# Kernel tuning notes

Hardware: AMD Instinct MI355X
Metric: run time of the kernel (lower is better)

Reference implementation:

```python
import jax, jax.numpy as jnp
import numpy as np

B, T, D, K = 256, 256, 768, 128  # batch, seq_len, num_dims, num_state


def setup_inputs() -> dict:
    key = jax.random.key(0)
    k1, k2, k3 = jax.random.split(key, 3)
    s = jax.random.normal(k1, (B, T, D), dtype=jnp.float32)          # embeddings
    means = jax.random.normal(k2, (K, D), dtype=jnp.float32)         # per-state Gaussian means
    var = jax.random.uniform(k3, (D,), dtype=jnp.float32,
                             minval=0.5, maxval=1.5)                  # shared diagonal variance
    return {"s": s, "means": means, "var": var}


def reference(s, means, var):
    """DMVFlow._eval_log_density: per-state diagonal-Gaussian log density.

    density[b,t,k] = -0.5*(D*log(2*pi) + sum_d log var[d])
                     -0.5*sum_d (s[b,t,d] - means[k,d])^2 / var[d]
    Expanded quadratic form so the k-contraction is a single GEMM instead of
    materializing a (B,T,K,D) broadcast.
    """
    d = s.shape[-1]
    inv_var = 1.0 / var                                              # (D,)
    log_norm = -0.5 * (d * jnp.log(2.0 * jnp.pi) + jnp.sum(jnp.log(var)))
    s2 = jnp.einsum('btd,d->bt', s * s, inv_var)                     # (B,T)
    cross = jnp.einsum('btd,kd->btk', s, means * inv_var)            # (B,T,K) GEMM
    m2 = jnp.einsum('kd,d->k', means * means, inv_var)               # (K,)
    quad = s2[..., None] - 2.0 * cross + m2                          # (B,T,K)
    return log_norm - 0.5 * quad
```

## Files before the change

### kernel.cpp

```cpp
#include <hip/hip_runtime.h>
#include <hip/hip_bf16.h>
#include <stdint.h>

#define D_DIM    768
#define K_STATES 128
#define M_ROWS   65536
#define BM       64
#define BK       32
#define NSTEPS   (D_DIM / BK)
#define LDSTRIDE 40

typedef __attribute__((ext_vector_type(8))) short bf16x8;
typedef __attribute__((ext_vector_type(4))) float f32x4;
typedef __attribute__((ext_vector_type(4))) int   i32x4;

__device__ __forceinline__ unsigned short f2bf(float f) {
    union { float f; unsigned u; } x; x.f = f;
    unsigned r = (x.u + 0x7FFFu + ((x.u >> 16) & 1u)) >> 16;
    return (unsigned short)r;
}

__global__ void __launch_bounds__(256) prep_kernel(
        const float* __restrict__ means, const float* __restrict__ var,
        unsigned short* __restrict__ mwbf, float* __restrict__ cvec) {
    const int k = blockIdx.x;
    const int t = threadIdx.x;
    float m2 = 0.f, ld = 0.f;
    for (int d = t; d < D_DIM; d += 256) {
        float v  = var[d];
        float iv = 1.0f / v;
        float m  = means[k * D_DIM + d];
        mwbf[k * D_DIM + d] = f2bf(m * iv);
        m2 += m * m * iv;
        ld += logf(v);
    }
#pragma unroll
    for (int off = 32; off > 0; off >>= 1) {
        m2 += __shfl_down(m2, off, 64);
        ld += __shfl_down(ld, off, 64);
    }
    __shared__ float rm[4], rl[4];
    const int wid = t >> 6;
    if ((t & 63) == 0) { rm[wid] = m2; rl[wid] = ld; }
    __syncthreads();
    if (t == 0) {
        float M2 = rm[0] + rm[1] + rm[2] + rm[3];
        float LD = rl[0] + rl[1] + rl[2] + rl[3];
        cvec[k] = -0.5f * ((float)D_DIM * 1.8378770664093453f + LD + M2);
    }
}

__global__ void __launch_bounds__(256, 4) dmv_main(
        const float* __restrict__ s, const unsigned short* __restrict__ mwbf,
        const float* __restrict__ var, const float* __restrict__ cvec,
        float* __restrict__ out) {
    __shared__ unsigned short As[2][BM * LDSTRIDE];
    __shared__ unsigned short Bs[2][K_STATES * LDSTRIDE];
    __shared__ float ivs[D_DIM];
    __shared__ float part[BM][8];
    __shared__ float s2row[BM];
    __shared__ float cs[K_STATES];

    const int t    = threadIdx.x;
    const int lane = t & 63;
    const int w    = t >> 6;
    const int wr   = w >> 1;
    const int wc   = w & 1;
    const long rowBase = (long)blockIdx.x * BM;

    for (int d = t; d < D_DIM; d += 256) ivs[d] = 1.0f / var[d];
    if (t < K_STATES) cs[t] = cvec[t];

    const int arow0 = t >> 3;
    const int acol  = (t & 7) * 4;
    const int brow0 = t >> 2;
    const int bcol  = (t & 3) * 8;

    const float*          sA = s    + (rowBase + arow0) * D_DIM + acol;
    const unsigned short* sB = mwbf + brow0 * D_DIM + bcol;

    f32x4 a0_[2], a1_[2];
    i32x4 b0_[2], b1_[2];
    float s2acc[2] = {0.f, 0.f};

    f32x4 acc[2][4];
#pragma unroll
    for (int i = 0; i < 2; ++i)
#pragma unroll
        for (int j = 0; j < 4; ++j) acc[i][j] = f32x4{0.f, 0.f, 0.f, 0.f};

#define LOADP(AP, BP, ST) do {                                                 \
    AP[0] = *(const f32x4*)(sA + (ST) * BK);                                   \
    AP[1] = *(const f32x4*)(sA + (long)32 * D_DIM + (ST) * BK);                \
    BP[0] = *(const i32x4*)(sB + (ST) * BK);                                   \
    BP[1] = *(const i32x4*)(sB + (long)64 * D_DIM + (ST) * BK);                \
} while (0)

#define STAGE(BUF, AP, BP, K0) do {                                            \
    f32x4 ivv = *reinterpret_cast<const f32x4*>(&ivs[(K0) + acol]);            \
    _Pragma("unroll")                                                          \
    for (int j = 0; j < 2; ++j) {                                              \
        const int row = j * 32 + arow0;                                        \
        f32x4 v = AP[j];                                                       \
        s2acc[j] += v[0]*v[0]*ivv[0] + v[1]*v[1]*ivv[1]                        \
                  + v[2]*v[2]*ivv[2] + v[3]*v[3]*ivv[3];                       \
        __hip_bfloat162 p0 = __float22bfloat162_rn(make_float2(v[0], v[1]));   \
        __hip_bfloat162 p1 = __float22bfloat162_rn(make_float2(v[2], v[3]));   \
        union { uint2 u2; __hip_bfloat162 h[2]; } pk;                          \
        pk.h[0] = p0; pk.h[1] = p1;                                            \
        *reinterpret_cast<uint2*>(&As[BUF][row * LDSTRIDE + acol]) = pk.u2;    \
    }                                                                          \
    _Pragma("unroll")                                                          \
    for (int j = 0; j < 2; ++j)                                                \
        *reinterpret_cast<i32x4*>(&Bs[BUF][(j * 64 + brow0) * LDSTRIDE + bcol])\
            = BP[j];                                                           \
} while (0)

    const int g  = (lane >> 4) * 8;
    const int rA = wr * 32 + (lane & 15);
    const int rB = wc * 64 + (lane & 15);

#define COMPUTE(BUF) do {                                                      \
    const unsigned short* Ab = &As[BUF][0];                                    \
    const unsigned short* Bb = &Bs[BUF][0];                                    \
    bf16x8 afrag[2], bfrag[4];                                                 \
    _Pragma("unroll")                                                          \
    for (int i = 0; i < 2; ++i)                                                \
        afrag[i] = *(const bf16x8*)(Ab + (rA + i * 16) * LDSTRIDE + g);        \
    _Pragma("unroll")                                                          \
    for (int j = 0; j < 4; ++j)                                                \
        bfrag[j] = *(const bf16x8*)(Bb + (rB + j * 16) * LDSTRIDE + g);        \
    _Pragma("unroll")                                                          \
    for (int i = 0; i < 2; ++i)                                                \
        _Pragma("unroll")                                                      \
        for (int j = 0; j < 4; ++j)                                            \
            acc[i][j] = __builtin_amdgcn_mfma_f32_16x16x32_bf16(               \
                            afrag[i], bfrag[j], acc[i][j], 0, 0, 0);           \
} while (0)

    LOADP(a0_, b0_, 0);
    LOADP(a1_, b1_, 1);
    __syncthreads();
    STAGE(0, a0_, b0_, 0);
    LOADP(a0_, b0_, 2);
    __syncthreads();

    for (int st = 0; st < NSTEPS; st += 2) {
        COMPUTE(0);
        STAGE(1, a1_, b1_, (st + 1) * BK);
        if (st + 3 < NSTEPS) LOADP(a1_, b1_, st + 3);
        __syncthreads();

        COMPUTE(1);
        if (st + 2 < NSTEPS) STAGE(0, a0_, b0_, (st + 2) * BK);
        if (st + 4 < NSTEPS) LOADP(a0_, b0_, st + 4);
        __syncthreads();
    }

#pragma unroll
    for (int j = 0; j < 2; ++j) part[j * 32 + arow0][t & 7] = s2acc[j];
    __syncthreads();
    if (t < BM) {
        float v = 0.f;
#pragma unroll
        for (int sl = 0; sl < 8; ++sl) v += part[t][sl];
        s2row[t] = v;
    }
    __syncthreads();

    const int colBase = wc * 64 + (lane & 15);
#pragma unroll
    for (int i = 0; i < 2; ++i) {
        const int rl0 = wr * 32 + i * 16 + (lane >> 4) * 4;
#pragma unroll
        for (int j = 0; j < 4; ++j) {
            const int col = colBase + j * 16;
            const float cj = cs[col];
#pragma unroll
            for (int r = 0; r < 4; ++r) {
                const int rl = rl0 + r;
                out[(rowBase + rl) * K_STATES + col] = acc[i][j][r] + cj - 0.5f * s2row[rl];
            }
        }
    }
#undef LOADP
#undef STAGE
#undef COMPUTE
}

extern "C" void kernel_launch(void* const* d_in, const int* in_sizes, int n_in,
                              void* d_out, int out_size, void* d_ws, size_t ws_size,
                              hipStream_t stream) {
    const float* s     = (const float*)d_in[0];
    const float* means = (const float*)d_in[1];
    const float* var   = (const float*)d_in[2];
    float* out = (float*)d_out;

    unsigned short* mwbf = (unsigned short*)d_ws;
    float* cvec = (float*)((char*)d_ws + (size_t)K_STATES * D_DIM * sizeof(unsigned short));

    prep_kernel<<<K_STATES, 256, 0, stream>>>(means, var, mwbf, cvec);
    dmv_main<<<M_ROWS / BM, 256, 0, stream>>>(s, mwbf, var, cvec, out);
}
```

Before: 46.02 us.

## Fuse means prep into GEMM kernel and single-buffer register prefetch

Removes the separate prep kernel. Each GEMM block now loads fp32 means directly, scales them by inverse variance, converts to bf16 in its staging step, and computes m2 and the log-variance constant itself. This saves a kernel launch and the workspace round trip. In exchange, all 1024 blocks redo the means scaling and read 4x more bytes for B (fp32 instead of bf16), and the prefetch depth drops from two register stages to one.

Result: slower. 52.98 us (+15.1%).

```diff
diff --git a/kernel.cpp b/kernel.cpp
--- a/kernel.cpp
+++ b/kernel.cpp
@@ -14,52 +14,16 @@
 typedef __attribute__((ext_vector_type(4))) float f32x4;
 typedef __attribute__((ext_vector_type(4))) int   i32x4;
 
-__device__ __forceinline__ unsigned short f2bf(float f) {
-    union { float f; unsigned u; } x; x.f = f;
-    unsigned r = (x.u + 0x7FFFu + ((x.u >> 16) & 1u)) >> 16;
-    return (unsigned short)r;
-}
-
-__global__ void __launch_bounds__(256) prep_kernel(
-        const float* __restrict__ means, const float* __restrict__ var,
-        unsigned short* __restrict__ mwbf, float* __restrict__ cvec) {
-    const int k = blockIdx.x;
-    const int t = threadIdx.x;
-    float m2 = 0.f, ld = 0.f;
-    for (int d = t; d < D_DIM; d += 256) {
-        float v  = var[d];
-        float iv = 1.0f / v;
-        float m  = means[k * D_DIM + d];
-        mwbf[k * D_DIM + d] = f2bf(m * iv);
-        m2 += m * m * iv;
-        ld += logf(v);
-    }
-#pragma unroll
-    for (int off = 32; off > 0; off >>= 1) {
-        m2 += __shfl_down(m2, off, 64);
-        ld += __shfl_down(ld, off, 64);
-    }
-    __shared__ float rm[4], rl[4];
-    const int wid = t >> 6;
-    if ((t & 63) == 0) { rm[wid] = m2; rl[wid] = ld; }
-    __syncthreads();
-    if (t == 0) {
-        float M2 = rm[0] + rm[1] + rm[2] + rm[3];
-        float LD = rl[0] + rl[1] + rl[2] + rl[3];
-        cvec[k] = -0.5f * ((float)D_DIM * 1.8378770664093453f + LD + M2);
-    }
-}
-
-__global__ void __launch_bounds__(256, 4) dmv_main(
-        const float* __restrict__ s, const unsigned short* __restrict__ mwbf,
-        const float* __restrict__ var, const float* __restrict__ cvec,
-        float* __restrict__ out) {
+__global__ void __launch_bounds__(256, 4) dmv_fused(
+        const float* __restrict__ s, const float* __restrict__ means,
+        const float* __restrict__ var, float* __restrict__ out) {
     __shared__ unsigned short As[2][BM * LDSTRIDE];
     __shared__ unsigned short Bs[2][K_STATES * LDSTRIDE];
     __shared__ float ivs[D_DIM];
     __shared__ float part[BM][8];
     __shared__ float s2row[BM];
     __shared__ float cs[K_STATES];
+    __shared__ float rlg[4];
 
     const int t    = threadIdx.x;
     const int lane = t & 63;
@@ -68,20 +32,28 @@
     const int wc   = w & 1;
     const long rowBase = (long)blockIdx.x * BM;
 
-    for (int d = t; d < D_DIM; d += 256) ivs[d] = 1.0f / var[d];
-    if (t < K_STATES) cs[t] = cvec[t];
+    float ldp = 0.f;
+    for (int d = t; d < D_DIM; d += 256) {
+        float v = var[d];
+        ivs[d] = 1.0f / v;
+        ldp += logf(v);
+    }
+#pragma unroll
+    for (int off = 32; off > 0; off >>= 1) ldp += __shfl_down(ldp, off, 64);
+    if ((t & 63) == 0) rlg[t >> 6] = ldp;
 
     const int arow0 = t >> 3;
     const int acol  = (t & 7) * 4;
-    const int brow0 = t >> 2;
-    const int bcol  = (t & 3) * 8;
+    const int brow  = t >> 1;
+    const int bcol0 = (t & 1) * 16;
 
-    const float*          sA = s    + (rowBase + arow0) * D_DIM + acol;
-    const unsigned short* sB = mwbf + brow0 * D_DIM + bcol;
+    const float* sA = s     + (rowBase + arow0) * D_DIM + acol;
+    const float* sM = means + brow * D_DIM + bcol0;
 
-    f32x4 a0_[2], a1_[2];
-    i32x4 b0_[2], b1_[2];
+    f32x4 aP[2];
+    f32x4 bP[4];
     float s2acc[2] = {0.f, 0.f};
+    float m2p = 0.f;
 
     f32x4 acc[2][4];
 #pragma unroll
@@ -89,31 +61,48 @@
 #pragma unroll
         for (int j = 0; j < 4; ++j) acc[i][j] = f32x4{0.f, 0.f, 0.f, 0.f};
 
-#define LOADP(AP, BP, ST) do {                                                 \
-    AP[0] = *(const f32x4*)(sA + (ST) * BK);                                   \
-    AP[1] = *(const f32x4*)(sA + (long)32 * D_DIM + (ST) * BK);                \
-    BP[0] = *(const i32x4*)(sB + (ST) * BK);                                   \
-    BP[1] = *(const i32x4*)(sB + (long)64 * D_DIM + (ST) * BK);                \
+#define LOADP(ST) do {                                                         \
+    aP[0] = *(const f32x4*)(sA + (ST) * BK);                                   \
+    aP[1] = *(const f32x4*)(sA + (long)32 * D_DIM + (ST) * BK);                \
+    bP[0] = *(const f32x4*)(sM + (ST) * BK);                                   \
+    bP[1] = *(const f32x4*)(sM + (ST) * BK + 4);                               \
+    bP[2] = *(const f32x4*)(sM + (ST) * BK + 8);                               \
+    bP[3] = *(const f32x4*)(sM + (ST) * BK + 12);                              \
 } while (0)
 
-#define STAGE(BUF, AP, BP, K0) do {                                            \
+#define STAGE(BUF, K0) do {                                                    \
+                                         \
     f32x4 ivv = *reinterpret_cast<const f32x4*>(&ivs[(K0) + acol]);            \
     _Pragma("unroll")                                                          \
     for (int j = 0; j < 2; ++j) {                                              \
         const int row = j * 32 + arow0;                                        \
-        f32x4 v = AP[j];                                                       \
+        f32x4 v = aP[j];                                                       \
         s2acc[j] += v[0]*v[0]*ivv[0] + v[1]*v[1]*ivv[1]                        \
                   + v[2]*v[2]*ivv[2] + v[3]*v[3]*ivv[3];                       \
-        __hip_bfloat162 p0 = __float22bfloat162_rn(make_float2(v[0], v[1]));   \
-        __hip_bfloat162 p1 = __float22bfloat162_rn(make_float2(v[2], v[3]));   \
         union { uint2 u2; __hip_bfloat162 h[2]; } pk;                          \
-        pk.h[0] = p0; pk.h[1] = p1;                                            \
+        pk.h[0] = __float22bfloat162_rn(make_float2(v[0], v[1]));              \
+        pk.h[1] = __float22bfloat162_rn(make_float2(v[2], v[3]));              \
         *reinterpret_cast<uint2*>(&As[BUF][row * LDSTRIDE + acol]) = pk.u2;    \
     }                                                                          \
-    _Pragma("unroll")                                                          \
-    for (int j = 0; j < 2; ++j)                                                \
-        *reinterpret_cast<i32x4*>(&Bs[BUF][(j * 64 + brow0) * LDSTRIDE + bcol])\
-            = BP[j];                                                           \
+                  \
+    {                                                                          \
+        union { i32x4 i4; __hip_bfloat162 h[4]; } q0, q1;                      \
+        _Pragma("unroll")                                                      \
+        for (int j = 0; j < 4; ++j) {                                          \
+            f32x4 iw = *reinterpret_cast<const f32x4*>(&ivs[(K0) + bcol0 + j*4]);\
+            f32x4 mv = bP[j];                                                  \
+            m2p += mv[0]*mv[0]*iw[0] + mv[1]*mv[1]*iw[1]                       \
+                 + mv[2]*mv[2]*iw[2] + mv[3]*mv[3]*iw[3];                      \
+            __hip_bfloat162 plo = __float22bfloat162_rn(                       \
+                make_float2(mv[0]*iw[0], mv[1]*iw[1]));                        \
+            __hip_bfloat162 phi = __float22bfloat162_rn(                       \
+                make_float2(mv[2]*iw[2], mv[3]*iw[3]));                        \
+            if (j < 2) { q0.h[(j&1)*2] = plo; q0.h[(j&1)*2+1] = phi; }         \
+            else       { q1.h[(j&1)*2] = plo; q1.h[(j&1)*2+1] = phi; }         \
+        }                                                                      \
+        *reinterpret_cast<i32x4*>(&Bs[BUF][brow * LDSTRIDE + bcol0])     = q0.i4;\
+        *reinterpret_cast<i32x4*>(&Bs[BUF][brow * LDSTRIDE + bcol0 + 8]) = q1.i4;\
+    }                                                                          \
 } while (0)
 
     const int g  = (lane >> 4) * 8;
@@ -138,27 +127,26 @@
                             afrag[i], bfrag[j], acc[i][j], 0, 0, 0);           \
 } while (0)
 
-    LOADP(a0_, b0_, 0);
-    LOADP(a1_, b1_, 1);
+    LOADP(0);
     __syncthreads();
-    STAGE(0, a0_, b0_, 0);
-    LOADP(a0_, b0_, 2);
-    __syncthreads();
+    const float slog = rlg[0] + rlg[1] + rlg[2] + rlg[3];
+    STAGE(0, 0);
 
-    for (int st = 0; st < NSTEPS; st += 2) {
-        COMPUTE(0);
-        STAGE(1, a1_, b1_, (st + 1) * BK);
-        if (st + 3 < NSTEPS) LOADP(a1_, b1_, st + 3);
+    for (int st = 0; st < NSTEPS; ++st) {
+        const int cur = st & 1;
+        if (st + 1 < NSTEPS) LOADP(st + 1);
         __syncthreads();
-
-        COMPUTE(1);
-        if (st + 2 < NSTEPS) STAGE(0, a0_, b0_, (st + 2) * BK);
-        if (st + 4 < NSTEPS) LOADP(a0_, b0_, st + 4);
-        __syncthreads();
+        COMPUTE(cur);
+        if (st + 1 < NSTEPS) STAGE(st + 1 & 1, (st + 1) * BK);
     }
 
 #pragma unroll
     for (int j = 0; j < 2; ++j) part[j * 32 + arow0][t & 7] = s2acc[j];
+    {
+        float m2t = m2p + __shfl_xor(m2p, 1, 64);
+        if (!(t & 1))
+            cs[brow] = -0.5f * ((float)D_DIM * 1.8378770664093453f + slog + m2t);
+    }
     __syncthreads();
     if (t < BM) {
         float v = 0.f;
@@ -196,9 +184,5 @@
     const float* var   = (const float*)d_in[2];
     float* out = (float*)d_out;
 
-    unsigned short* mwbf = (unsigned short*)d_ws;
-    float* cvec = (float*)((char*)d_ws + (size_t)K_STATES * D_DIM * sizeof(unsigned short));
-
-    prep_kernel<<<K_STATES, 256, 0, stream>>>(means, var, mwbf, cvec);
-    dmv_main<<<M_ROWS / BM, 256, 0, stream>>>(s, mwbf, var, cvec, out);
+    dmv_fused<<<M_ROWS / BM, 256, 0, stream>>>(s, means, var, out);
 }
```

## Double K-tile depth and simplify to one-barrier-per-step register prefetch pipeline

Applied to the files above, without the earlier changes.

Raises the reduction tile from 32 to 64 columns, with a padded LDS stride of 72. This halves the number of main-loop steps and barriers, and each COMPUTE now issues two MFMA k-substeps. The two-register-set prefetch scheme is replaced by a single prefetch buffer, one barrier per step, and a new thread-to-element mapping in which each thread loads four contiguous 16-byte chunks per row. Launch bounds drop from 4 to 2 blocks per SM, and the LDS footprint roughly doubles. On a kernel close to memory-bandwidth bound, this fewer-but-larger-step scheme may cost latency hiding.

Result: slower. 48.33 us (+5.0%).

```diff
diff --git a/kernel.cpp b/kernel.cpp
--- a/kernel.cpp
+++ b/kernel.cpp
@@ -6,9 +6,9 @@
 #define K_STATES 128
 #define M_ROWS   65536
 #define BM       64
-#define BK       32
+#define BK       64
 #define NSTEPS   (D_DIM / BK)
-#define LDSTRIDE 40
+#define LDSTRIDE 72
 
 typedef __attribute__((ext_vector_type(8))) short bf16x8;
 typedef __attribute__((ext_vector_type(4))) float f32x4;
@@ -50,14 +50,14 @@
     }
 }
 
-__global__ void __launch_bounds__(256, 4) dmv_main(
+__global__ void __launch_bounds__(256, 2) dmv_main(
         const float* __restrict__ s, const unsigned short* __restrict__ mwbf,
         const float* __restrict__ var, const float* __restrict__ cvec,
         float* __restrict__ out) {
     __shared__ unsigned short As[2][BM * LDSTRIDE];
     __shared__ unsigned short Bs[2][K_STATES * LDSTRIDE];
     __shared__ float ivs[D_DIM];
-    __shared__ float part[BM][8];
+    __shared__ float part[BM][4];
     __shared__ float s2row[BM];
     __shared__ float cs[K_STATES];
 
@@ -71,17 +71,17 @@
     for (int d = t; d < D_DIM; d += 256) ivs[d] = 1.0f / var[d];
     if (t < K_STATES) cs[t] = cvec[t];
 
-    const int arow0 = t >> 3;
-    const int acol  = (t & 7) * 4;
-    const int brow0 = t >> 2;
-    const int bcol  = (t & 3) * 8;
+    const int arow = t >> 2;
+    const int acol = (t & 3) * 4;
+    const int brow = t >> 1;
+    const int bcol = (t & 1) * 32;
 
-    const float*          sA = s    + (rowBase + arow0) * D_DIM + acol;
-    const unsigned short* sB = mwbf + brow0 * D_DIM + bcol;
+    const float*          sA = s    + (rowBase + arow) * D_DIM + acol;
+    const unsigned short* sB = mwbf + brow * D_DIM + bcol;
 
-    f32x4 a0_[2], a1_[2];
-    i32x4 b0_[2], b1_[2];
-    float s2acc[2] = {0.f, 0.f};
+    f32x4 aP[4];
+    i32x4 bP[4];
+    float s2acc = 0.f;
 
     f32x4 acc[2][4];
 #pragma unroll
@@ -89,31 +89,32 @@
 #pragma unroll
         for (int j = 0; j < 4; ++j) acc[i][j] = f32x4{0.f, 0.f, 0.f, 0.f};
 
-#define LOADP(AP, BP, ST) do {                                                 \
-    AP[0] = *(const f32x4*)(sA + (ST) * BK);                                   \
-    AP[1] = *(const f32x4*)(sA + (long)32 * D_DIM + (ST) * BK);                \
-    BP[0] = *(const i32x4*)(sB + (ST) * BK);                                   \
-    BP[1] = *(const i32x4*)(sB + (long)64 * D_DIM + (ST) * BK);                \
+#define LOADP(ST) do {                                                         \
+    _Pragma("unroll")                                                          \
+    for (int j = 0; j < 4; ++j)                                                \
+        aP[j] = *(const f32x4*)(sA + (ST) * BK + j * 16);                      \
+    _Pragma("unroll")                                                          \
+    for (int j = 0; j < 4; ++j)                                                \
+        bP[j] = *(const i32x4*)(sB + (ST) * BK + j * 8);                       \
 } while (0)
 
-#define STAGE(BUF, AP, BP, K0) do {                                            \
-    f32x4 ivv = *reinterpret_cast<const f32x4*>(&ivs[(K0) + acol]);            \
+#define STAGE(BUF, K0) do {                                                    \
     _Pragma("unroll")                                                          \
-    for (int j = 0; j < 2; ++j) {                                              \
-        const int row = j * 32 + arow0;                                        \
-        f32x4 v = AP[j];                                                       \
-        s2acc[j] += v[0]*v[0]*ivv[0] + v[1]*v[1]*ivv[1]                        \
-                  + v[2]*v[2]*ivv[2] + v[3]*v[3]*ivv[3];                       \
-        __hip_bfloat162 p0 = __float22bfloat162_rn(make_float2(v[0], v[1]));   \
-        __hip_bfloat162 p1 = __float22bfloat162_rn(make_float2(v[2], v[3]));   \
+    for (int j = 0; j < 4; ++j) {                                              \
+        f32x4 ivv = *reinterpret_cast<const f32x4*>(&ivs[(K0) + j * 16 + acol]);\
+        f32x4 v = aP[j];                                                       \
+        s2acc += v[0]*v[0]*ivv[0] + v[1]*v[1]*ivv[1]                           \
+               + v[2]*v[2]*ivv[2] + v[3]*v[3]*ivv[3];                          \
         union { uint2 u2; __hip_bfloat162 h[2]; } pk;                          \
-        pk.h[0] = p0; pk.h[1] = p1;                                            \
-        *reinterpret_cast<uint2*>(&As[BUF][row * LDSTRIDE + acol]) = pk.u2;    \
+        pk.h[0] = __float22bfloat162_rn(make_float2(v[0], v[1]));              \
+        pk.h[1] = __float22bfloat162_rn(make_float2(v[2], v[3]));              \
+        *reinterpret_cast<uint2*>(&As[BUF][arow * LDSTRIDE + j * 16 + acol])   \
+            = pk.u2;                                                           \
     }                                                                          \
     _Pragma("unroll")                                                          \
-    for (int j = 0; j < 2; ++j)                                                \
-        *reinterpret_cast<i32x4*>(&Bs[BUF][(j * 64 + brow0) * LDSTRIDE + bcol])\
-            = BP[j];                                                           \
+    for (int j = 0; j < 4; ++j)                                                \
+        *reinterpret_cast<i32x4*>(&Bs[BUF][brow * LDSTRIDE + bcol + j * 8])    \
+            = bP[j];                                                           \
 } while (0)
 
     const int g  = (lane >> 4) * 8;
@@ -123,49 +124,42 @@
 #define COMPUTE(BUF) do {                                                      \
     const unsigned short* Ab = &As[BUF][0];                                    \
     const unsigned short* Bb = &Bs[BUF][0];                                    \
-    bf16x8 afrag[2], bfrag[4];                                                 \
     _Pragma("unroll")                                                          \
-    for (int i = 0; i < 2; ++i)                                                \
-        afrag[i] = *(const bf16x8*)(Ab + (rA + i * 16) * LDSTRIDE + g);        \
-    _Pragma("unroll")                                                          \
-    for (int j = 0; j < 4; ++j)                                                \
-        bfrag[j] = *(const bf16x8*)(Bb + (rB + j * 16) * LDSTRIDE + g);        \
-    _Pragma("unroll")                                                          \
-    for (int i = 0; i < 2; ++i)                                                \
+    for (int ks = 0; ks < 2; ++ks) {                                           \
+        bf16x8 afrag[2], bfrag[4];                                             \
+        _Pragma("unroll")                                                      \
+        for (int i = 0; i < 2; ++i)                                            \
+            afrag[i] = *(const bf16x8*)(Ab + (rA + i * 16) * LDSTRIDE          \
+                                           + ks * 32 + g);                     \
         _Pragma("unroll")                                                      \
         for (int j = 0; j < 4; ++j)                                            \
-            acc[i][j] = __builtin_amdgcn_mfma_f32_16x16x32_bf16(               \
-                            afrag[i], bfrag[j], acc[i][j], 0, 0, 0);           \
+            bfrag[j] = *(const bf16x8*)(Bb + (rB + j * 16) * LDSTRIDE          \
+                                           + ks * 32 + g);                     \
+        _Pragma("unroll")                                                      \
+        for (int i = 0; i < 2; ++i)                                            \
+            _Pragma("unroll")                                                  \
+            for (int j = 0; j < 4; ++j)                                        \
+                acc[i][j] = __builtin_amdgcn_mfma_f32_16x16x32_bf16(           \
+                                afrag[i], bfrag[j], acc[i][j], 0, 0, 0);       \
+    }                                                                          \
 } while (0)
 
-    LOADP(a0_, b0_, 0);
-    LOADP(a1_, b1_, 1);
+    LOADP(0);
     __syncthreads();
-    STAGE(0, a0_, b0_, 0);
-    LOADP(a0_, b0_, 2);
-    __syncthreads();
+    STAGE(0, 0);
 
-    for (int st = 0; st < NSTEPS; st += 2) {
-        COMPUTE(0);
-        STAGE(1, a1_, b1_, (st + 1) * BK);
-        if (st + 3 < NSTEPS) LOADP(a1_, b1_, st + 3);
+    for (int st = 0; st < NSTEPS; ++st) {
+        const int cur = st & 1;
+        if (st + 1 < NSTEPS) LOADP(st + 1);
         __syncthreads();
-
-        COMPUTE(1);
-        if (st + 2 < NSTEPS) STAGE(0, a0_, b0_, (st + 2) * BK);
-        if (st + 4 < NSTEPS) LOADP(a0_, b0_, st + 4);
-        __syncthreads();
+        COMPUTE(cur);
+        if (st + 1 < NSTEPS) STAGE((st + 1) & 1, (st + 1) * BK);
     }
 
-#pragma unroll
-    for (int j = 0; j < 2; ++j) part[j * 32 + arow0][t & 7] = s2acc[j];
+    part[arow][t & 3] = s2acc;
     __syncthreads();
-    if (t < BM) {
-        float v = 0.f;
-#pragma unroll
-        for (int sl = 0; sl < 8; ++sl) v += part[t][sl];
-        s2row[t] = v;
-    }
+    if (t < BM)
+        s2row[t] = part[t][0] + part[t][1] + part[t][2] + part[t][3];
     __syncthreads();
 
     const int colBase = wc * 64 + (lane & 15);
```
